# Kernel tuning notes

Hardware: AMD Instinct MI355X
Metric: run time of the kernel (lower is better)

## Reference

```python
import jax, jax.numpy as jnp
import numpy as np

D = 512      # d_model
H = 8        # num_heads
HD = D // H  # head_dim = 64 (concat makes per-head dim 2*HD=128)
B = 32       # batch*group
T = 512      # time steps


def setup_inputs() -> dict:
    key = jax.random.key(0)
    ks = jax.random.split(key, 18)
    def W(k):
        return jax.random.normal(k, (D, D), dtype=jnp.float32) * 0.02
    inp = {
        "x_face": jax.random.normal(ks[0], (B, T, D), dtype=jnp.float32),
        "x_skeleton": jax.random.normal(ks[1], (B, T, D), dtype=jnp.float32),
        "wq1": W(ks[2]), "bq1": jnp.zeros((D,), jnp.float32),
        "wk1": W(ks[3]), "bk1": jnp.zeros((D,), jnp.float32),
        "wv1": W(ks[4]), "bv1": jnp.zeros((D,), jnp.float32),
        "wq2": W(ks[5]), "bq2": jnp.zeros((D,), jnp.float32),
        "wk2": W(ks[6]), "bk2": jnp.zeros((D,), jnp.float32),
        "wv2": W(ks[7]), "bv2": jnp.zeros((D,), jnp.float32),
        "wo1": W(ks[8]), "bo1": jnp.zeros((D,), jnp.float32),
        "wo2": W(ks[9]), "bo2": jnp.zeros((D,), jnp.float32),
    }
    return inp


def reference(x_face, x_skeleton,
              wq1, bq1, wk1, bk1, wv1, bv1,
              wq2, bq2, wk2, bk2, wv2, bv2,
              wo1, bo1, wo2, bo2):
    Bt, Tt, _ = x_face.shape

    def proj(x, w, b):
        # torch Linear: x @ W^T + b, then 'b t (h d) -> b h t d'
        return (x @ w.T + b).reshape(Bt, Tt, H, HD).transpose(0, 2, 1, 3)

    q = jnp.concatenate([proj(x_face, wq1, bq1), proj(x_skeleton, wq2, bq2)], axis=3)  # [B,H,T,2*HD]
    k = jnp.concatenate([proj(x_face, wk1, bk1), proj(x_skeleton, wk2, bk2)], axis=3)
    v = jnp.concatenate([proj(x_face, wv1, bv1), proj(x_skeleton, wv2, bv2)], axis=3)

    scores = jnp.einsum('bhid,bhjd->bhij', q, k) / (HD ** 0.5)  # scale by head_dim**0.5 as in source
    attn = jax.nn.softmax(scores, axis=-1)                      # dropout = identity (eval mode)
    out = jnp.einsum('bhij,bhjd->bhid', attn, v)                # [B,H,T,2*HD]
    out = out.transpose(0, 2, 1, 3).reshape(Bt, Tt, 2 * D)      # 'b h t d -> b t (h d)'

    x1, x2 = out[..., :D], out[..., D:]
    return (x1 @ wo1.T + bo1, x2 @ wo2.T + bo2)
```

## Files before the change

kernel.cpp:

```cpp
#include <hip/hip_runtime.h>
#include <hip/hip_bf16.h>
#include <stdint.h>

typedef __hip_bfloat16 bf16;
using f32x4 = __attribute__((ext_vector_type(4))) float;
using s16x8 = __attribute__((ext_vector_type(8))) short;

typedef __attribute__((address_space(1))) unsigned int gu32;
typedef __attribute__((address_space(3))) unsigned int lu32;

__device__ __forceinline__ void gll16(const void* g, void* l) {
  __builtin_amdgcn_global_load_lds((const gu32*)g, (lu32*)l, 16, 0, 0);
}

struct ConvJob { const float* src; bf16* dst; int n4; int pad; };
struct ConvParams { ConvJob j[10]; };
struct alignas(8) Bf4 { bf16 v[4]; };

__global__ void convert_kernel(ConvParams p) {
  ConvJob jb = p.j[blockIdx.z];
  int stride = gridDim.x * blockDim.x;
  for (int i = blockIdx.x * blockDim.x + threadIdx.x; i < jb.n4; i += stride) {
    float4 v = ((const float4*)jb.src)[i];
    Bf4 o;
    o.v[0] = __float2bfloat16(v.x);
    o.v[1] = __float2bfloat16(v.y);
    o.v[2] = __float2bfloat16(v.z);
    o.v[3] = __float2bfloat16(v.w);
    ((Bf4*)jb.dst)[i] = o;
  }
}

struct GemmSlice {
  const bf16* A; const bf16* W; const float* bias;
  bf16* dstQ; float* dstF;
  long lda; int dhalf; float scale; int mode;
};
struct GemmParams { GemmSlice s[6]; };

#define GSTAGE(kb, bA, bB) do { \
    _Pragma("unroll") \
    for (int i_ = 0; i_ < 4; ++i_) { \
      const int r0_ = w * 32 + i_ * 8; \
      gll16(Abase + (long)r0_ * lda + (kb) * 64, (bA) + r0_ * 64); \
      gll16(Wbase + (long)r0_ * 512 + (kb) * 64, (bB) + r0_ * 64); \
    } \
  } while (0)

#define GCOMPUTE(bA, bB) do { \
  _Pragma("unroll") \
  for (int ks = 0; ks < 2; ++ks) { \
    s16x8 af[4], bg[4]; \
    _Pragma("unroll") \
    for (int mi = 0; mi < 4; ++mi) { \
      const int row_ = wm + mi * 16 + fr; \
      af[mi] = *(const s16x8*)((bA) + row_ * 64 + ((ks * 32 + fq * 8) ^ ((row_ & 7) << 3))); \
    } \
    _Pragma("unroll") \
    for (int ni = 0; ni < 4; ++ni) { \
      const int row_ = wn + ni * 16 + fr; \
      bg[ni] = *(const s16x8*)((bB) + row_ * 64 + ((ks * 32 + fq * 8) ^ ((row_ & 7) << 3))); \
    } \
    __builtin_amdgcn_s_setprio(1); \
    _Pragma("unroll") \
    for (int mi = 0; mi < 4; ++mi) \
      _Pragma("unroll") \
      for (int ni = 0; ni < 4; ++ni) \
        acc[mi][ni] = __builtin_amdgcn_mfma_f32_16x16x32_bf16(af[mi], bg[ni], acc[mi][ni], 0, 0, 0); \
    __builtin_amdgcn_s_setprio(0); \
  } \
} while (0)

__global__ __launch_bounds__(256, 2) void gemm_kernel(GemmParams p) {
  __shared__ alignas(16) bf16 lds[4 * 8192];
  bf16* const sA0 = lds;
  bf16* const sB0 = lds + 8192;
  bf16* const sA1 = lds + 16384;
  bf16* const sB1 = lds + 24576;
  const GemmSlice sl = p.s[blockIdx.z];
  const long lda = sl.lda;
  const int tid = threadIdx.x;
  const int w = tid >> 6, ln = tid & 63;
  const int gm0 = blockIdx.x * 128;
  const int gn0 = blockIdx.y * 128;
  const int arow = ln >> 3;
  const int acolS = ((ln & 7) ^ (ln >> 3)) * 8;
  const int wm = (w >> 1) * 64, wn = (w & 1) * 64;
  const int fr = ln & 15, fq = ln >> 4;
  const bf16* const Abase = sl.A + (long)(gm0 + arow) * lda + acolS;
  const bf16* const Wbase = sl.W + (long)(gn0 + arow) * 512 + acolS;
  f32x4 acc[4][4] = {};

  GSTAGE(0, sA0, sB0);
  GSTAGE(1, sA1, sB1);

  for (int kt = 0; kt < 7; ++kt) {
    bf16* const bA = (kt & 1) ? sA1 : sA0;
    bf16* const bB = (kt & 1) ? sB1 : sB0;
    asm volatile("s_waitcnt vmcnt(8)" ::: "memory");
    __builtin_amdgcn_sched_barrier(0);
    __builtin_amdgcn_s_barrier();
    GCOMPUTE(bA, bB);
    asm volatile("s_waitcnt lgkmcnt(0)" ::: "memory");
    __builtin_amdgcn_sched_barrier(0);
    __builtin_amdgcn_s_barrier();
    if (kt < 6) GSTAGE(kt + 2, bA, bB);
  }
  asm volatile("s_waitcnt vmcnt(0)" ::: "memory");
  __builtin_amdgcn_sched_barrier(0);
  __builtin_amdgcn_s_barrier();
  GCOMPUTE(sA1, sB1);

  asm volatile("s_waitcnt lgkmcnt(0)" ::: "memory");
  __builtin_amdgcn_sched_barrier(0);
  __builtin_amdgcn_s_barrier();

  bf16* const eW = lds + w * 4608;
  if (sl.mode == 0) {
    const int col0 = gn0 + wn;
    const int h = col0 >> 6;
    const int bh = ((gm0 >> 9) << 3) + h;
    const int tb = (gm0 & 511) + wm;
#pragma unroll
    for (int ni = 0; ni < 4; ++ni) {
      const float bia = sl.bias[col0 + ni * 16 + fr];
#pragma unroll
      for (int mi = 0; mi < 4; ++mi)
#pragma unroll
        for (int r = 0; r < 4; ++r)
          eW[(mi * 16 + fq * 4 + r) * 72 + ni * 16 + fr] =
              __float2bfloat16((acc[mi][ni][r] + bia) * sl.scale);
    }
#pragma unroll
    for (int pp = 0; pp < 8; ++pp) {
      const int rr = pp * 8 + (ln >> 3);
      const s16x8 v = *(const s16x8*)(eW + rr * 72 + (ln & 7) * 8);
      *(s16x8*)(sl.dstQ + (((long)bh * 512 + tb + rr) << 7) + sl.dhalf + (ln & 7) * 8) = v;
    }
  } else if (sl.mode == 2) {
    const int col0 = gn0 + wn;
    const int h = col0 >> 6;
    const int bh = ((gm0 >> 9) << 3) + h;
    const int tb = (gm0 & 511) + wm;
#pragma unroll
    for (int ni = 0; ni < 4; ++ni) {
      const float bia = sl.bias[col0 + ni * 16 + fr];
#pragma unroll
      for (int mi = 0; mi < 4; ++mi) {
        Bf4 o;
#pragma unroll
        for (int r = 0; r < 4; ++r) o.v[r] = __float2bfloat16(acc[mi][ni][r] + bia);
        *(Bf4*)(eW + (ni * 16 + fr) * 72 + mi * 16 + fq * 4) = o;
      }
    }
#pragma unroll
    for (int pp = 0; pp < 8; ++pp) {
      const int rr = pp * 8 + (ln >> 3);
      const s16x8 v = *(const s16x8*)(eW + rr * 72 + (ln & 7) * 8);
      *(s16x8*)(sl.dstQ + (((long)bh * 128 + sl.dhalf + rr) << 9) + tb + (ln & 7) * 8) = v;
    }
  } else {
#pragma unroll
    for (int mi = 0; mi < 4; ++mi)
#pragma unroll
      for (int ni = 0; ni < 4; ++ni) {
        const int col = gn0 + wn + ni * 16 + fr;
        const float bia = sl.bias[col];
#pragma unroll
        for (int r = 0; r < 4; ++r) {
          const int row = gm0 + wm + mi * 16 + fq * 4 + r;
          sl.dstF[(long)row * 512 + col] = acc[mi][ni][r] + bia;
        }
      }
  }
}

#define STAGE(kt, bK, bV) do { \
    _Pragma("unroll") \
    for (int p_ = 0; p_ < 4; ++p_) \
      gll16(kgb + (kt) * 8192 + p_ * 2048, (bK) + tid * 8 + p_ * 2048); \
    _Pragma("unroll") \
    for (int p_ = 0; p_ < 4; ++p_) \
      gll16(vgb + (kt) * 64 + p_ * 16384, (bV) + tid * 8 + p_ * 2048); \
  } while (0)

#define COMPUTE(bK, bV) do { \
  f32x4 s2[2][4] = {}; \
  _Pragma("unroll") \
  for (int ks = 0; ks < 4; ++ks) { \
    _Pragma("unroll") \
    for (int ni = 0; ni < 4; ++ni) { \
      const int row_ = ni * 16 + fr; \
      const s16x8 kf = *(const s16x8*)((bK) + row_ * 128 + ((ks * 32 + fq * 8) ^ ((row_ & 7) << 3))); \
      _Pragma("unroll") \
      for (int mi = 0; mi < 2; ++mi) \
        s2[mi][ni] = __builtin_amdgcn_mfma_f32_16x16x32_bf16(qf[mi][ks], kf, s2[mi][ni], 0, 0, 0); \
    } \
  } \
  _Pragma("unroll") \
  for (int mi = 0; mi < 2; ++mi) \
    _Pragma("unroll") \
    for (int r = 0; r < 4; ++r) { \
      float ps = 0.f; \
      _Pragma("unroll") \
      for (int ni = 0; ni < 4; ++ni) { \
        const float pe = __builtin_amdgcn_exp2f(s2[mi][ni][r]); \
        s2[mi][ni][r] = pe; ps += pe; \
      } \
      ps += __shfl_xor(ps, 1); ps += __shfl_xor(ps, 2); \
      ps += __shfl_xor(ps, 4); ps += __shfl_xor(ps, 8); \
      lrow[mi][r] += ps; \
    } \
  _Pragma("unroll") \
  for (int mi = 0; mi < 2; ++mi) \
    _Pragma("unroll") \
    for (int ni = 0; ni < 4; ++ni) \
      _Pragma("unroll") \
      for (int r = 0; r < 4; ++r) { \
        const int rp = mi * 16 + fq * 4 + r; \
        sPw[rp * 64 + ((ni * 16 + fr) ^ ((rp & 7) << 3))] = __float2bfloat16(s2[mi][ni][r]); \
      } \
  _Pragma("unroll") \
  for (int ks = 0; ks < 2; ++ks) { \
    s16x8 pf[2]; \
    _Pragma("unroll") \
    for (int mi = 0; mi < 2; ++mi) { \
      const int row_ = mi * 16 + fr; \
      pf[mi] = *(const s16x8*)(sPw + row_ * 64 + ((ks * 32 + fq * 8) ^ ((row_ & 7) << 3))); \
    } \
    _Pragma("unroll") \
    for (int nj = 0; nj < 8; ++nj) { \
      const int row_ = nj * 16 + fr; \
      const s16x8 vf = *(const s16x8*)((bV) + row_ * 64 + ((ks * 32 + fq * 8) ^ ((row_ & 7) << 3))); \
      _Pragma("unroll") \
      for (int mi = 0; mi < 2; ++mi) \
        o[mi][nj] = __builtin_amdgcn_mfma_f32_16x16x32_bf16(pf[mi], vf, o[mi][nj], 0, 0, 0); \
    } \
  } \
} while (0)

__global__ __launch_bounds__(256, 2) void attn_kernel(const bf16* __restrict__ Q,
                                                      const bf16* __restrict__ K,
                                                      const bf16* __restrict__ Vt,
                                                      bf16* __restrict__ AO) {
  __shared__ alignas(16) bf16 lds[40960];
  bf16* const ldsK0 = lds;
  bf16* const ldsV0 = lds + 8192;
  bf16* const ldsK1 = lds + 16384;
  bf16* const ldsV1 = lds + 24576;
  bf16* const sP    = lds + 32768;
  const int tid = threadIdx.x;
  const int w = tid >> 6, ln = tid & 63;
  const int fr = ln & 15, fq = ln >> 4;
  const int lg = (blockIdx.x & 7) * 128 + (blockIdx.x >> 3);
  const int bh = lg >> 2;
  const int q0 = (lg & 3) * 128;
  const long base = (long)bh << 16;
  bf16* const sPw = sP + w * 2048;

  const int kr0 = tid >> 4, kc = tid & 15;
  const int vr0 = tid >> 3, vc = tid & 7;
  const bf16* const kgb = K + base + kr0 * 128 + ((kc ^ (kr0 & 7)) * 8);
  const bf16* const vgb = Vt + base + (long)vr0 * 512 + ((vc ^ (vr0 & 7)) * 8);

  {
    const bf16* const qgb = Q + base + (long)q0 * 128 + kr0 * 128 + ((kc ^ (kr0 & 7)) * 8);
#pragma unroll
    for (int p = 0; p < 8; ++p)
      gll16(qgb + p * 2048, lds + tid * 8 + p * 2048);
  }
  __syncthreads();
  s16x8 qf[2][4];
#pragma unroll
  for (int mi = 0; mi < 2; ++mi) {
    const int row = w * 32 + mi * 16 + fr;
#pragma unroll
    for (int ks = 0; ks < 4; ++ks)
      qf[mi][ks] = *(const s16x8*)(lds + row * 128 + ((ks * 32 + fq * 8) ^ ((row & 7) << 3)));
  }
  __syncthreads();

  f32x4 o[2][8] = {};
  float lrow[2][4] = {};

  STAGE(0, ldsK0, ldsV0);
  STAGE(1, ldsK1, ldsV1);

  for (int kt = 0; kt < 7; ++kt) {
    const bf16* bK = (kt & 1) ? ldsK1 : ldsK0;
    const bf16* bV = (kt & 1) ? ldsV1 : ldsV0;
    asm volatile("s_waitcnt vmcnt(8)" ::: "memory");
    __builtin_amdgcn_sched_barrier(0);
    __builtin_amdgcn_s_barrier();
    COMPUTE(bK, bV);
    asm volatile("s_waitcnt lgkmcnt(0)" ::: "memory");
    __builtin_amdgcn_sched_barrier(0);
    __builtin_amdgcn_s_barrier();
    if (kt < 6) STAGE(kt + 2, (bf16*)bK, (bf16*)bV);
  }
  asm volatile("s_waitcnt vmcnt(0)" ::: "memory");
  __builtin_amdgcn_sched_barrier(0);
  __builtin_amdgcn_s_barrier();
  COMPUTE(ldsK1, ldsV1);

  const int b = bh >> 3, h = bh & 7;
  float rl[2][4];
#pragma unroll
  for (int mi = 0; mi < 2; ++mi)
#pragma unroll
    for (int r = 0; r < 4; ++r) rl[mi][r] = 1.f / lrow[mi][r];
#pragma unroll
  for (int mi = 0; mi < 2; ++mi)
#pragma unroll
    for (int nj = 0; nj < 8; ++nj) {
      const int col = h * 128 + nj * 16 + fr;
#pragma unroll
      for (int r = 0; r < 4; ++r) {
        const int trow = q0 + w * 32 + mi * 16 + fq * 4 + r;
        AO[((long)(b * 512 + trow) << 10) + col] = __float2bfloat16(o[mi][nj][r] * rl[mi][r]);
      }
    }
}

extern "C" void kernel_launch(void* const* d_in, const int* in_sizes, int n_in,
                              void* d_out, int out_size, void* d_ws, size_t ws_size,
                              hipStream_t stream) {
  const float* xf = (const float*)d_in[0];
  const float* xs = (const float*)d_in[1];
  const float* w_f[8] = { (const float*)d_in[2], (const float*)d_in[4], (const float*)d_in[6],
                          (const float*)d_in[8], (const float*)d_in[10], (const float*)d_in[12],
                          (const float*)d_in[14], (const float*)d_in[16] };

  bf16* ws = (bf16*)d_ws;
  bf16* XF = ws;
  bf16* XS = ws + 8388608;
  bf16* WW = ws + 16777216;
  bf16* Qb = ws + 18874368;
  bf16* Kb = Qb + 16777216;
  bf16* Vb = Kb + 16777216;
  bf16* AO = ws;

  ConvParams cp;
  cp.j[0] = { xf, XF, 2097152, 0 };
  cp.j[1] = { xs, XS, 2097152, 0 };
  for (int i = 0; i < 8; ++i) cp.j[2 + i] = { w_f[i], WW + i * 262144, 65536, 0 };
  convert_kernel<<<dim3(512, 1, 10), 256, 0, stream>>>(cp);

  const float qsc = 0.125f * 1.44269504088896f;
  GemmParams gp;
  gp.s[0] = { XF, WW + 0 * 262144, (const float*)d_in[3],  Qb, nullptr, 512, 0,  qsc, 0 };
  gp.s[1] = { XS, WW + 3 * 262144, (const float*)d_in[9],  Qb, nullptr, 512, 64, qsc, 0 };
  gp.s[2] = { XF, WW + 1 * 262144, (const float*)d_in[5],  Kb, nullptr, 512, 0,  1.f, 0 };
  gp.s[3] = { XS, WW + 4 * 262144, (const float*)d_in[11], Kb, nullptr, 512, 64, 1.f, 0 };
  gp.s[4] = { XF, WW + 2 * 262144, (const float*)d_in[7],  Vb, nullptr, 512, 0,  1.f, 2 };
  gp.s[5] = { XS, WW + 5 * 262144, (const float*)d_in[13], Vb, nullptr, 512, 64, 1.f, 2 };
  gemm_kernel<<<dim3(128, 4, 6), 256, 0, stream>>>(gp);

  attn_kernel<<<dim3(1024), 256, 0, stream>>>(Qb, Kb, Vb, AO);

  float* out = (float*)d_out;
  GemmParams op;
  op.s[0] = { AO,       WW + 6 * 262144, (const float*)d_in[15], nullptr, out,           1024, 0, 1.f, 1 };
  op.s[1] = { AO + 512, WW + 7 * 262144, (const float*)d_in[17], nullptr, out + 8388608, 1024, 0, 1.f, 1 };
  op.s[2] = op.s[0]; op.s[3] = op.s[0]; op.s[4] = op.s[0]; op.s[5] = op.s[0];
  gemm_kernel<<<dim3(128, 4, 2), 256, 0, stream>>>(op);
}
```

Before: 173.1 us.

## Load K/V fragments directly from global memory, dropping LDS double-buffering in attention

```diff
diff --git a/kernel.cpp b/kernel.cpp
--- a/kernel.cpp
+++ b/kernel.cpp
@@ -175,80 +175,11 @@
   }
 }
 
-#define STAGE(kt, bK, bV) do { \
-    _Pragma("unroll") \
-    for (int p_ = 0; p_ < 4; ++p_) \
-      gll16(kgb + (kt) * 8192 + p_ * 2048, (bK) + tid * 8 + p_ * 2048); \
-    _Pragma("unroll") \
-    for (int p_ = 0; p_ < 4; ++p_) \
-      gll16(vgb + (kt) * 64 + p_ * 16384, (bV) + tid * 8 + p_ * 2048); \
-  } while (0)
-
-#define COMPUTE(bK, bV) do { \
-  f32x4 s2[2][4] = {}; \
-  _Pragma("unroll") \
-  for (int ks = 0; ks < 4; ++ks) { \
-    _Pragma("unroll") \
-    for (int ni = 0; ni < 4; ++ni) { \
-      const int row_ = ni * 16 + fr; \
-      const s16x8 kf = *(const s16x8*)((bK) + row_ * 128 + ((ks * 32 + fq * 8) ^ ((row_ & 7) << 3))); \
-      _Pragma("unroll") \
-      for (int mi = 0; mi < 2; ++mi) \
-        s2[mi][ni] = __builtin_amdgcn_mfma_f32_16x16x32_bf16(qf[mi][ks], kf, s2[mi][ni], 0, 0, 0); \
-    } \
-  } \
-  _Pragma("unroll") \
-  for (int mi = 0; mi < 2; ++mi) \
-    _Pragma("unroll") \
-    for (int r = 0; r < 4; ++r) { \
-      float ps = 0.f; \
-      _Pragma("unroll") \
-      for (int ni = 0; ni < 4; ++ni) { \
-        const float pe = __builtin_amdgcn_exp2f(s2[mi][ni][r]); \
-        s2[mi][ni][r] = pe; ps += pe; \
-      } \
-      ps += __shfl_xor(ps, 1); ps += __shfl_xor(ps, 2); \
-      ps += __shfl_xor(ps, 4); ps += __shfl_xor(ps, 8); \
-      lrow[mi][r] += ps; \
-    } \
-  _Pragma("unroll") \
-  for (int mi = 0; mi < 2; ++mi) \
-    _Pragma("unroll") \
-    for (int ni = 0; ni < 4; ++ni) \
-      _Pragma("unroll") \
-      for (int r = 0; r < 4; ++r) { \
-        const int rp = mi * 16 + fq * 4 + r; \
-        sPw[rp * 64 + ((ni * 16 + fr) ^ ((rp & 7) << 3))] = __float2bfloat16(s2[mi][ni][r]); \
-      } \
-  _Pragma("unroll") \
-  for (int ks = 0; ks < 2; ++ks) { \
-    s16x8 pf[2]; \
-    _Pragma("unroll") \
-    for (int mi = 0; mi < 2; ++mi) { \
-      const int row_ = mi * 16 + fr; \
-      pf[mi] = *(const s16x8*)(sPw + row_ * 64 + ((ks * 32 + fq * 8) ^ ((row_ & 7) << 3))); \
-    } \
-    _Pragma("unroll") \
-    for (int nj = 0; nj < 8; ++nj) { \
-      const int row_ = nj * 16 + fr; \
-      const s16x8 vf = *(const s16x8*)((bV) + row_ * 64 + ((ks * 32 + fq * 8) ^ ((row_ & 7) << 3))); \
-      _Pragma("unroll") \
-      for (int mi = 0; mi < 2; ++mi) \
-        o[mi][nj] = __builtin_amdgcn_mfma_f32_16x16x32_bf16(pf[mi], vf, o[mi][nj], 0, 0, 0); \
-    } \
-  } \
-} while (0)
-
-__global__ __launch_bounds__(256, 2) void attn_kernel(const bf16* __restrict__ Q,
+__global__ __launch_bounds__(256, 4) void attn_kernel(const bf16* __restrict__ Q,
                                                       const bf16* __restrict__ K,
                                                       const bf16* __restrict__ Vt,
                                                       bf16* __restrict__ AO) {
-  __shared__ alignas(16) bf16 lds[40960];
-  bf16* const ldsK0 = lds;
-  bf16* const ldsV0 = lds + 8192;
-  bf16* const ldsK1 = lds + 16384;
-  bf16* const ldsV1 = lds + 24576;
-  bf16* const sP    = lds + 32768;
+  __shared__ alignas(16) bf16 sP[8192];
   const int tid = threadIdx.x;
   const int w = tid >> 6, ln = tid & 63;
   const int fr = ln & 15, fq = ln >> 4;
@@ -258,50 +189,72 @@
   const long base = (long)bh << 16;
   bf16* const sPw = sP + w * 2048;
 
-  const int kr0 = tid >> 4, kc = tid & 15;
-  const int vr0 = tid >> 3, vc = tid & 7;
-  const bf16* const kgb = K + base + kr0 * 128 + ((kc ^ (kr0 & 7)) * 8);
-  const bf16* const vgb = Vt + base + (long)vr0 * 512 + ((vc ^ (vr0 & 7)) * 8);
-
-  {
-    const bf16* const qgb = Q + base + (long)q0 * 128 + kr0 * 128 + ((kc ^ (kr0 & 7)) * 8);
-#pragma unroll
-    for (int p = 0; p < 8; ++p)
-      gll16(qgb + p * 2048, lds + tid * 8 + p * 2048);
-  }
-  __syncthreads();
   s16x8 qf[2][4];
 #pragma unroll
   for (int mi = 0; mi < 2; ++mi) {
-    const int row = w * 32 + mi * 16 + fr;
+    const long qrow = base + (long)(q0 + w * 32 + mi * 16 + fr) * 128;
 #pragma unroll
     for (int ks = 0; ks < 4; ++ks)
-      qf[mi][ks] = *(const s16x8*)(lds + row * 128 + ((ks * 32 + fq * 8) ^ ((row & 7) << 3)));
-  }
-  __syncthreads();
+      qf[mi][ks] = *(const s16x8*)(Q + qrow + ks * 32 + fq * 8);
+  }
 
   f32x4 o[2][8] = {};
   float lrow[2][4] = {};
 
-  STAGE(0, ldsK0, ldsV0);
-  STAGE(1, ldsK1, ldsV1);
-
-  for (int kt = 0; kt < 7; ++kt) {
-    const bf16* bK = (kt & 1) ? ldsK1 : ldsK0;
-    const bf16* bV = (kt & 1) ? ldsV1 : ldsV0;
-    asm volatile("s_waitcnt vmcnt(8)" ::: "memory");
-    __builtin_amdgcn_sched_barrier(0);
-    __builtin_amdgcn_s_barrier();
-    COMPUTE(bK, bV);
-    asm volatile("s_waitcnt lgkmcnt(0)" ::: "memory");
-    __builtin_amdgcn_sched_barrier(0);
-    __builtin_amdgcn_s_barrier();
-    if (kt < 6) STAGE(kt + 2, (bf16*)bK, (bf16*)bV);
-  }
-  asm volatile("s_waitcnt vmcnt(0)" ::: "memory");
-  __builtin_amdgcn_sched_barrier(0);
-  __builtin_amdgcn_s_barrier();
-  COMPUTE(ldsK1, ldsV1);
+  for (int kt = 0; kt < 8; ++kt) {
+    f32x4 s2[2][4] = {};
+#pragma unroll
+    for (int ks = 0; ks < 4; ++ks) {
+      s16x8 kf[4];
+#pragma unroll
+      for (int ni = 0; ni < 4; ++ni)
+        kf[ni] = *(const s16x8*)(K + base + (long)(kt * 64 + ni * 16 + fr) * 128 + ks * 32 + fq * 8);
+#pragma unroll
+      for (int ni = 0; ni < 4; ++ni)
+#pragma unroll
+        for (int mi = 0; mi < 2; ++mi)
+          s2[mi][ni] = __builtin_amdgcn_mfma_f32_16x16x32_bf16(qf[mi][ks], kf[ni], s2[mi][ni], 0, 0, 0);
+    }
+#pragma unroll
+    for (int mi = 0; mi < 2; ++mi)
+#pragma unroll
+      for (int r = 0; r < 4; ++r) {
+        float ps = 0.f;
+#pragma unroll
+        for (int ni = 0; ni < 4; ++ni) {
+          const float pe = __builtin_amdgcn_exp2f(s2[mi][ni][r]);
+          s2[mi][ni][r] = pe; ps += pe;
+        }
+        ps += __shfl_xor(ps, 1); ps += __shfl_xor(ps, 2);
+        ps += __shfl_xor(ps, 4); ps += __shfl_xor(ps, 8);
+        lrow[mi][r] += ps;
+      }
+#pragma unroll
+    for (int mi = 0; mi < 2; ++mi)
+#pragma unroll
+      for (int ni = 0; ni < 4; ++ni)
+#pragma unroll
+        for (int r = 0; r < 4; ++r) {
+          const int rp = mi * 16 + fq * 4 + r;
+          sPw[rp * 64 + ((ni * 16 + fr) ^ ((rp & 7) << 3))] = __float2bfloat16(s2[mi][ni][r]);
+        }
+#pragma unroll
+    for (int ks2 = 0; ks2 < 2; ++ks2) {
+      s16x8 pf[2];
+#pragma unroll
+      for (int mi = 0; mi < 2; ++mi) {
+        const int row_ = mi * 16 + fr;
+        pf[mi] = *(const s16x8*)(sPw + row_ * 64 + ((ks2 * 32 + fq * 8) ^ ((row_ & 7) << 3)));
+      }
+#pragma unroll
+      for (int nj = 0; nj < 8; ++nj) {
+        const s16x8 vf = *(const s16x8*)(Vt + base + (long)(nj * 16 + fr) * 512 + kt * 64 + ks2 * 32 + fq * 8);
+#pragma unroll
+        for (int mi = 0; mi < 2; ++mi)
+          o[mi][nj] = __builtin_amdgcn_mfma_f32_16x16x32_bf16(pf[mi], vf, o[mi][nj], 0, 0, 0);
+      }
+    }
+  }
 
   const int b = bh >> 3, h = bh & 7;
   float rl[2][4];
@@ -310,16 +263,24 @@
 #pragma unroll
     for (int r = 0; r < 4; ++r) rl[mi][r] = 1.f / lrow[mi][r];
 #pragma unroll
-  for (int mi = 0; mi < 2; ++mi)
-#pragma unroll
-    for (int nj = 0; nj < 8; ++nj) {
-      const int col = h * 128 + nj * 16 + fr;
-#pragma unroll
-      for (int r = 0; r < 4; ++r) {
-        const int trow = q0 + w * 32 + mi * 16 + fq * 4 + r;
-        AO[((long)(b * 512 + trow) << 10) + col] = __float2bfloat16(o[mi][nj][r] * rl[mi][r]);
-      }
-    }
+  for (int hh = 0; hh < 2; ++hh) {
+#pragma unroll
+    for (int mi = 0; mi < 2; ++mi)
+#pragma unroll
+      for (int nj4 = 0; nj4 < 4; ++nj4)
+#pragma unroll
+        for (int r = 0; r < 4; ++r) {
+          const int rp = mi * 16 + fq * 4 + r;
+          sPw[rp * 64 + ((nj4 * 16 + fr) ^ ((rp & 7) << 3))] =
+              __float2bfloat16(o[mi][hh * 4 + nj4][r] * rl[mi][r]);
+        }
+#pragma unroll
+    for (int pp = 0; pp < 4; ++pp) {
+      const int rr = pp * 8 + (ln >> 3);
+      const s16x8 v = *(const s16x8*)(sPw + rr * 64 + (((ln & 7) * 8) ^ ((rr & 7) << 3)));
+      *(s16x8*)(AO + (((long)(b * 512 + q0 + w * 32 + rr)) << 10) + h * 128 + hh * 64 + (ln & 7) * 8) = v;
+    }
+  }
 }
 
 extern "C" void kernel_launch(void* const* d_in, const int* in_sizes, int n_in,
```

Measured after the change: 342.5 us. 97.8% more time.

## Single-buffer attention LDS with register prefetch and vectorized output stores

Applied to the files above, without the earlier changes.

```diff
diff --git a/kernel.cpp b/kernel.cpp
--- a/kernel.cpp
+++ b/kernel.cpp
@@ -175,23 +175,37 @@
   }
 }
 
-#define STAGE(kt, bK, bV) do { \
+#define STAGE(kt) do { \
     _Pragma("unroll") \
     for (int p_ = 0; p_ < 4; ++p_) \
-      gll16(kgb + (kt) * 8192 + p_ * 2048, (bK) + tid * 8 + p_ * 2048); \
+      gll16(kgb + (kt) * 8192 + p_ * 2048, ldsK + tid * 8 + p_ * 2048); \
     _Pragma("unroll") \
     for (int p_ = 0; p_ < 4; ++p_) \
-      gll16(vgb + (kt) * 64 + p_ * 16384, (bV) + tid * 8 + p_ * 2048); \
+      gll16(vgb + (kt) * 64 + p_ * 16384, ldsV + tid * 8 + p_ * 2048); \
   } while (0)
 
-#define COMPUTE(bK, bV) do { \
+#define LOADR(kt) do { \
+    _Pragma("unroll") \
+    for (int p_ = 0; p_ < 4; ++p_) kreg[p_] = *(const s16x8*)(kgb + (kt) * 8192 + p_ * 2048); \
+    _Pragma("unroll") \
+    for (int p_ = 0; p_ < 4; ++p_) vreg[p_] = *(const s16x8*)(vgb + (kt) * 64 + p_ * 16384); \
+  } while (0)
+
+#define WRITER() do { \
+    _Pragma("unroll") \
+    for (int p_ = 0; p_ < 4; ++p_) *(s16x8*)(ldsK + tid * 8 + p_ * 2048) = kreg[p_]; \
+    _Pragma("unroll") \
+    for (int p_ = 0; p_ < 4; ++p_) *(s16x8*)(ldsV + tid * 8 + p_ * 2048) = vreg[p_]; \
+  } while (0)
+
+#define COMPUTE() do { \
   f32x4 s2[2][4] = {}; \
   _Pragma("unroll") \
   for (int ks = 0; ks < 4; ++ks) { \
     _Pragma("unroll") \
     for (int ni = 0; ni < 4; ++ni) { \
       const int row_ = ni * 16 + fr; \
-      const s16x8 kf = *(const s16x8*)((bK) + row_ * 128 + ((ks * 32 + fq * 8) ^ ((row_ & 7) << 3))); \
+      const s16x8 kf = *(const s16x8*)(ldsK + row_ * 128 + ((ks * 32 + fq * 8) ^ ((row_ & 7) << 3))); \
       _Pragma("unroll") \
       for (int mi = 0; mi < 2; ++mi) \
         s2[mi][ni] = __builtin_amdgcn_mfma_f32_16x16x32_bf16(qf[mi][ks], kf, s2[mi][ni], 0, 0, 0); \
@@ -231,7 +245,7 @@
     _Pragma("unroll") \
     for (int nj = 0; nj < 8; ++nj) { \
       const int row_ = nj * 16 + fr; \
-      const s16x8 vf = *(const s16x8*)((bV) + row_ * 64 + ((ks * 32 + fq * 8) ^ ((row_ & 7) << 3))); \
+      const s16x8 vf = *(const s16x8*)(ldsV + row_ * 64 + ((ks * 32 + fq * 8) ^ ((row_ & 7) << 3))); \
       _Pragma("unroll") \
       for (int mi = 0; mi < 2; ++mi) \
         o[mi][nj] = __builtin_amdgcn_mfma_f32_16x16x32_bf16(pf[mi], vf, o[mi][nj], 0, 0, 0); \
@@ -239,16 +253,14 @@
   } \
 } while (0)
 
-__global__ __launch_bounds__(256, 2) void attn_kernel(const bf16* __restrict__ Q,
+__global__ __launch_bounds__(256, 3) void attn_kernel(const bf16* __restrict__ Q,
                                                       const bf16* __restrict__ K,
                                                       const bf16* __restrict__ Vt,
                                                       bf16* __restrict__ AO) {
-  __shared__ alignas(16) bf16 lds[40960];
-  bf16* const ldsK0 = lds;
-  bf16* const ldsV0 = lds + 8192;
-  bf16* const ldsK1 = lds + 16384;
-  bf16* const ldsV1 = lds + 24576;
-  bf16* const sP    = lds + 32768;
+  __shared__ alignas(16) bf16 lds[24576];
+  bf16* const ldsK = lds;
+  bf16* const ldsV = lds + 8192;
+  bf16* const sP   = lds + 16384;
   const int tid = threadIdx.x;
   const int w = tid >> 6, ln = tid & 63;
   const int fr = ln & 15, fq = ln >> 4;
@@ -282,26 +294,29 @@
 
   f32x4 o[2][8] = {};
   float lrow[2][4] = {};
-
-  STAGE(0, ldsK0, ldsV0);
-  STAGE(1, ldsK1, ldsV1);
-
-  for (int kt = 0; kt < 7; ++kt) {
-    const bf16* bK = (kt & 1) ? ldsK1 : ldsK0;
-    const bf16* bV = (kt & 1) ? ldsV1 : ldsV0;
-    asm volatile("s_waitcnt vmcnt(8)" ::: "memory");
-    __builtin_amdgcn_sched_barrier(0);
-    __builtin_amdgcn_s_barrier();
-    COMPUTE(bK, bV);
+  s16x8 kreg[4], vreg[4];
+
+  STAGE(0);
+  __builtin_amdgcn_sched_barrier(0);
+  LOADR(1);
+  __builtin_amdgcn_sched_barrier(0);
+  asm volatile("s_waitcnt vmcnt(8)" ::: "memory");
+  __builtin_amdgcn_sched_barrier(0);
+  __builtin_amdgcn_s_barrier();
+
+  for (int kt = 0; kt < 8; ++kt) {
+    COMPUTE();
     asm volatile("s_waitcnt lgkmcnt(0)" ::: "memory");
     __builtin_amdgcn_sched_barrier(0);
     __builtin_amdgcn_s_barrier();
-    if (kt < 6) STAGE(kt + 2, (bf16*)bK, (bf16*)bV);
-  }
-  asm volatile("s_waitcnt vmcnt(0)" ::: "memory");
-  __builtin_amdgcn_sched_barrier(0);
-  __builtin_amdgcn_s_barrier();
-  COMPUTE(ldsK1, ldsV1);
+    if (kt < 7) {
+      WRITER();
+      if (kt < 6) LOADR(kt + 2);
+      asm volatile("s_waitcnt lgkmcnt(0)" ::: "memory");
+      __builtin_amdgcn_sched_barrier(0);
+      __builtin_amdgcn_s_barrier();
+    }
+  }
 
   const int b = bh >> 3, h = bh & 7;
   float rl[2][4];
@@ -310,16 +325,24 @@
 #pragma unroll
     for (int r = 0; r < 4; ++r) rl[mi][r] = 1.f / lrow[mi][r];
 #pragma unroll
-  for (int mi = 0; mi < 2; ++mi)
-#pragma unroll
-    for (int nj = 0; nj < 8; ++nj) {
-      const int col = h * 128 + nj * 16 + fr;
-#pragma unroll
-      for (int r = 0; r < 4; ++r) {
-        const int trow = q0 + w * 32 + mi * 16 + fq * 4 + r;
-        AO[((long)(b * 512 + trow) << 10) + col] = __float2bfloat16(o[mi][nj][r] * rl[mi][r]);
-      }
-    }
+  for (int hh = 0; hh < 2; ++hh) {
+#pragma unroll
+    for (int mi = 0; mi < 2; ++mi)
+#pragma unroll
+      for (int nj4 = 0; nj4 < 4; ++nj4)
+#pragma unroll
+        for (int r = 0; r < 4; ++r) {
+          const int rp = mi * 16 + fq * 4 + r;
+          sPw[rp * 64 + ((nj4 * 16 + fr) ^ ((rp & 7) << 3))] =
+              __float2bfloat16(o[mi][hh * 4 + nj4][r] * rl[mi][r]);
+        }
+#pragma unroll
+    for (int pp = 0; pp < 4; ++pp) {
+      const int rr = pp * 8 + (ln >> 3);
+      const s16x8 v = *(const s16x8*)(sPw + rr * 64 + (((ln & 7) * 8) ^ ((rr & 7) << 3)));
+      *(s16x8*)(AO + (((long)(b * 512 + q0 + w * 32 + rr)) << 10) + h * 128 + hh * 64 + (ln & 7) * 8) = v;
+    }
+  }
 }
 
 extern "C" void kernel_launch(void* const* d_in, const int* in_sizes, int n_in,
```

Result: slower. 348.6 us (+101.4%).

## Single-buffer GEMM LDS for higher occupancy and stage attention output through LDS

Applied to the files above, without the earlier changes.

```diff
diff --git a/kernel.cpp b/kernel.cpp
--- a/kernel.cpp
+++ b/kernel.cpp
@@ -38,28 +38,28 @@
 };
 struct GemmParams { GemmSlice s[6]; };
 
-#define GSTAGE(kb, bA, bB) do { \
+#define GSTAGE(kb) do { \
     _Pragma("unroll") \
     for (int i_ = 0; i_ < 4; ++i_) { \
       const int r0_ = w * 32 + i_ * 8; \
-      gll16(Abase + (long)r0_ * lda + (kb) * 64, (bA) + r0_ * 64); \
-      gll16(Wbase + (long)r0_ * 512 + (kb) * 64, (bB) + r0_ * 64); \
+      gll16(Abase + (long)r0_ * lda + (kb) * 64, sA + r0_ * 64); \
+      gll16(Wbase + (long)r0_ * 512 + (kb) * 64, sB + r0_ * 64); \
     } \
   } while (0)
 
-#define GCOMPUTE(bA, bB) do { \
+#define GCOMPUTE() do { \
   _Pragma("unroll") \
   for (int ks = 0; ks < 2; ++ks) { \
     s16x8 af[4], bg[4]; \
     _Pragma("unroll") \
     for (int mi = 0; mi < 4; ++mi) { \
       const int row_ = wm + mi * 16 + fr; \
-      af[mi] = *(const s16x8*)((bA) + row_ * 64 + ((ks * 32 + fq * 8) ^ ((row_ & 7) << 3))); \
+      af[mi] = *(const s16x8*)(sA + row_ * 64 + ((ks * 32 + fq * 8) ^ ((row_ & 7) << 3))); \
     } \
     _Pragma("unroll") \
     for (int ni = 0; ni < 4; ++ni) { \
       const int row_ = wn + ni * 16 + fr; \
-      bg[ni] = *(const s16x8*)((bB) + row_ * 64 + ((ks * 32 + fq * 8) ^ ((row_ & 7) << 3))); \
+      bg[ni] = *(const s16x8*)(sB + row_ * 64 + ((ks * 32 + fq * 8) ^ ((row_ & 7) << 3))); \
     } \
     __builtin_amdgcn_s_setprio(1); \
     _Pragma("unroll") \
@@ -71,12 +71,10 @@
   } \
 } while (0)
 
-__global__ __launch_bounds__(256, 2) void gemm_kernel(GemmParams p) {
-  __shared__ alignas(16) bf16 lds[4 * 8192];
-  bf16* const sA0 = lds;
-  bf16* const sB0 = lds + 8192;
-  bf16* const sA1 = lds + 16384;
-  bf16* const sB1 = lds + 24576;
+__global__ __launch_bounds__(256, 4) void gemm_kernel(GemmParams p) {
+  __shared__ alignas(16) bf16 lds[16384];
+  bf16* const sA = lds;
+  bf16* const sB = lds + 8192;
   const GemmSlice sl = p.s[blockIdx.z];
   const long lda = sl.lda;
   const int tid = threadIdx.x;
@@ -91,51 +89,39 @@
   const bf16* const Wbase = sl.W + (long)(gn0 + arow) * 512 + acolS;
   f32x4 acc[4][4] = {};
 
-  GSTAGE(0, sA0, sB0);
-  GSTAGE(1, sA1, sB1);
-
-  for (int kt = 0; kt < 7; ++kt) {
-    bf16* const bA = (kt & 1) ? sA1 : sA0;
-    bf16* const bB = (kt & 1) ? sB1 : sB0;
-    asm volatile("s_waitcnt vmcnt(8)" ::: "memory");
-    __builtin_amdgcn_sched_barrier(0);
-    __builtin_amdgcn_s_barrier();
-    GCOMPUTE(bA, bB);
-    asm volatile("s_waitcnt lgkmcnt(0)" ::: "memory");
-    __builtin_amdgcn_sched_barrier(0);
-    __builtin_amdgcn_s_barrier();
-    if (kt < 6) GSTAGE(kt + 2, bA, bB);
-  }
-  asm volatile("s_waitcnt vmcnt(0)" ::: "memory");
-  __builtin_amdgcn_sched_barrier(0);
-  __builtin_amdgcn_s_barrier();
-  GCOMPUTE(sA1, sB1);
-
-  asm volatile("s_waitcnt lgkmcnt(0)" ::: "memory");
-  __builtin_amdgcn_sched_barrier(0);
-  __builtin_amdgcn_s_barrier();
-
-  bf16* const eW = lds + w * 4608;
+  for (int kb = 0; kb < 8; ++kb) {
+    GSTAGE(kb);
+    __syncthreads();
+    GCOMPUTE();
+    __syncthreads();
+  }
+
+  bf16* const eW = lds + w * 2304;
   if (sl.mode == 0) {
     const int col0 = gn0 + wn;
     const int h = col0 >> 6;
     const int bh = ((gm0 >> 9) << 3) + h;
     const int tb = (gm0 & 511) + wm;
 #pragma unroll
-    for (int ni = 0; ni < 4; ++ni) {
-      const float bia = sl.bias[col0 + ni * 16 + fr];
-#pragma unroll
-      for (int mi = 0; mi < 4; ++mi)
-#pragma unroll
-        for (int r = 0; r < 4; ++r)
-          eW[(mi * 16 + fq * 4 + r) * 72 + ni * 16 + fr] =
-              __float2bfloat16((acc[mi][ni][r] + bia) * sl.scale);
-    }
-#pragma unroll
-    for (int pp = 0; pp < 8; ++pp) {
-      const int rr = pp * 8 + (ln >> 3);
-      const s16x8 v = *(const s16x8*)(eW + rr * 72 + (ln & 7) * 8);
-      *(s16x8*)(sl.dstQ + (((long)bh * 512 + tb + rr) << 7) + sl.dhalf + (ln & 7) * 8) = v;
+    for (int ps = 0; ps < 2; ++ps) {
+#pragma unroll
+      for (int mi2 = 0; mi2 < 2; ++mi2) {
+        const int mi = ps * 2 + mi2;
+#pragma unroll
+        for (int ni = 0; ni < 4; ++ni) {
+          const float bia = sl.bias[col0 + ni * 16 + fr];
+#pragma unroll
+          for (int r = 0; r < 4; ++r)
+            eW[(mi2 * 16 + fq * 4 + r) * 72 + ni * 16 + fr] =
+                __float2bfloat16((acc[mi][ni][r] + bia) * sl.scale);
+        }
+      }
+#pragma unroll
+      for (int pp = 0; pp < 4; ++pp) {
+        const int rr = pp * 8 + (ln >> 3);
+        const s16x8 v = *(const s16x8*)(eW + rr * 72 + (ln & 7) * 8);
+        *(s16x8*)(sl.dstQ + (((long)bh * 512 + tb + ps * 32 + rr) << 7) + sl.dhalf + (ln & 7) * 8) = v;
+      }
     }
   } else if (sl.mode == 2) {
     const int col0 = gn0 + wn;
@@ -143,21 +129,25 @@
     const int bh = ((gm0 >> 9) << 3) + h;
     const int tb = (gm0 & 511) + wm;
 #pragma unroll
-    for (int ni = 0; ni < 4; ++ni) {
-      const float bia = sl.bias[col0 + ni * 16 + fr];
-#pragma unroll
-      for (int mi = 0; mi < 4; ++mi) {
-        Bf4 o;
-#pragma unroll
-        for (int r = 0; r < 4; ++r) o.v[r] = __float2bfloat16(acc[mi][ni][r] + bia);
-        *(Bf4*)(eW + (ni * 16 + fr) * 72 + mi * 16 + fq * 4) = o;
-      }
-    }
-#pragma unroll
-    for (int pp = 0; pp < 8; ++pp) {
-      const int rr = pp * 8 + (ln >> 3);
-      const s16x8 v = *(const s16x8*)(eW + rr * 72 + (ln & 7) * 8);
-      *(s16x8*)(sl.dstQ + (((long)bh * 128 + sl.dhalf + rr) << 9) + tb + (ln & 7) * 8) = v;
+    for (int ps = 0; ps < 2; ++ps) {
+#pragma unroll
+      for (int ni2 = 0; ni2 < 2; ++ni2) {
+        const int ni = ps * 2 + ni2;
+        const float bia = sl.bias[col0 + ni * 16 + fr];
+#pragma unroll
+        for (int mi = 0; mi < 4; ++mi) {
+          Bf4 o;
+#pragma unroll
+          for (int r = 0; r < 4; ++r) o.v[r] = __float2bfloat16(acc[mi][ni][r] + bia);
+          *(Bf4*)(eW + (ni2 * 16 + fr) * 72 + mi * 16 + fq * 4) = o;
+        }
+      }
+#pragma unroll
+      for (int pp = 0; pp < 4; ++pp) {
+        const int rr = pp * 8 + (ln >> 3);
+        const s16x8 v = *(const s16x8*)(eW + rr * 72 + (ln & 7) * 8);
+        *(s16x8*)(sl.dstQ + (((long)bh * 128 + sl.dhalf + ps * 32 + rr) << 9) + tb + (ln & 7) * 8) = v;
+      }
     }
   } else {
 #pragma unroll
@@ -310,16 +300,24 @@
 #pragma unroll
     for (int r = 0; r < 4; ++r) rl[mi][r] = 1.f / lrow[mi][r];
 #pragma unroll
-  for (int mi = 0; mi < 2; ++mi)
-#pragma unroll
-    for (int nj = 0; nj < 8; ++nj) {
-      const int col = h * 128 + nj * 16 + fr;
-#pragma unroll
-      for (int r = 0; r < 4; ++r) {
-        const int trow = q0 + w * 32 + mi * 16 + fq * 4 + r;
-        AO[((long)(b * 512 + trow) << 10) + col] = __float2bfloat16(o[mi][nj][r] * rl[mi][r]);
-      }
+  for (int hh = 0; hh < 2; ++hh) {
+#pragma unroll
+    for (int mi = 0; mi < 2; ++mi)
+#pragma unroll
+      for (int nj4 = 0; nj4 < 4; ++nj4)
+#pragma unroll
+        for (int r = 0; r < 4; ++r) {
+          const int rp = mi * 16 + fq * 4 + r;
+          sPw[rp * 64 + ((nj4 * 16 + fr) ^ ((rp & 7) << 3))] =
+              __float2bfloat16(o[mi][hh * 4 + nj4][r] * rl[mi][r]);
+        }
+#pragma unroll
+    for (int pp = 0; pp < 4; ++pp) {
+      const int rr = pp * 8 + (ln >> 3);
+      const s16x8 v = *(const s16x8*)(sPw + rr * 64 + (((ln & 7) * 8) ^ ((rr & 7) << 3)));
+      *(s16x8*)(AO + (((long)(b * 512 + q0 + w * 32 + rr)) << 10) + h * 128 + hh * 64 + (ln & 7) * 8) = v;
     }
+  }
 }
 
 extern "C" void kernel_launch(void* const* d_in, const int* in_sizes, int n_in,
```

Result: faster. 163.4 us (-5.6%).
